# Performance work log

Hardware: AMD Instinct MI355X
Metric: run time of the kernel (lower is better)

## Reference

```python
import jax, jax.numpy as jnp
import numpy as np

N_ATOMS = 20000
N_EDGES = 500000
F = 128


def setup_inputs() -> dict:
    key = jax.random.key(0)
    ks = jax.random.split(key, 10)
    q = jax.random.normal(ks[0], (N_ATOMS, 1, F), dtype=jnp.float32)
    mu = jax.random.normal(ks[1], (N_ATOMS, 3, F), dtype=jnp.float32)
    Wij = jax.random.normal(ks[2], (N_EDGES, 1, 3 * F), dtype=jnp.float32)
    dir_ij = jax.random.normal(ks[3], (N_EDGES, 3), dtype=jnp.float32)
    idx_i = jax.random.randint(ks[4], (N_EDGES,), 0, N_ATOMS)
    idx_j = jax.random.randint(ks[5], (N_EDGES,), 0, N_ATOMS)
    # interatomic_context_net params: Dense(F->F, silu), Dense(F->3F)
    W1 = jax.random.normal(ks[6], (F, F), dtype=jnp.float32) * 0.05
    b1 = jnp.zeros((F,), dtype=jnp.float32)
    W2 = jax.random.normal(ks[7], (F, 3 * F), dtype=jnp.float32) * 0.05
    b2 = jnp.zeros((3 * F,), dtype=jnp.float32)
    return {"q": q, "mu": mu, "Wij": Wij, "dir_ij": dir_ij,
            "idx_i": idx_i, "idx_j": idx_j, "n_atoms": N_ATOMS,
            "W1": W1, "b1": b1, "W2": W2, "b2": b2}


def reference(q, mu, Wij, dir_ij, idx_i, idx_j, n_atoms, W1, b1, W2, b2):
    nb = q.shape[-1]  # n_atom_basis
    # interatomic_context_net: Dense(silu) -> Dense(linear)
    h = jax.nn.silu(jnp.einsum('naf,fg->nag', q, W1) + b1)
    x = jnp.einsum('naf,fg->nag', h, W2) + b2            # [N, 1, 3F]
    # gather to edges, apply radial filter
    x = Wij * x[idx_j]                                   # [E, 1, 3F]
    dq, dmuR, dmumu = jnp.split(x, 3, axis=-1)           # each [E, 1, F]
    dq = jax.ops.segment_sum(dq, idx_i, num_segments=n_atoms)       # [N, 1, F]
    muj = mu[idx_j]                                      # [E, 3, F]
    dmu = dmuR * dir_ij[..., None] + dmumu * muj         # [E, 3, F]
    dmu = jax.ops.segment_sum(dmu, idx_i, num_segments=n_atoms)     # [N, 3, F]
    return q + dq, mu + dmu
```

## Files before the change

### kernel.cpp

```cpp
#include <hip/hip_runtime.h>
#include <hip/hip_bf16.h>

#define N_ATOMS 20000
#define N_EDGES 500000
#define FDIM    128
#define TFDIM   384

__device__ inline float4 ld4(const float* p) { return *(const float4*)p; }
__device__ inline void st4(float* p, float4 v) { *(float4*)p = v; }
__device__ inline float4 mul4(float4 a, float4 b) {
    return make_float4(a.x*b.x, a.y*b.y, a.z*b.z, a.w*b.w);
}
__device__ inline void fma4(float4& acc, float4 a, float4 b) {
    acc.x += a.x*b.x; acc.y += a.y*b.y; acc.z += a.z*b.z; acc.w += a.w*b.w;
}
__device__ inline void fma4s(float4& acc, float4 a, float s) {
    acc.x += a.x*s; acc.y += a.y*s; acc.z += a.z*s; acc.w += a.w*s;
}


__global__ void zero_counts_kernel(int* __restrict__ counts) {
    int i = blockIdx.x * 256 + threadIdx.x;
    if (i < N_ATOMS) counts[i] = 0;
}

__global__ void hist_kernel(const int* __restrict__ idx_i, int* __restrict__ counts) {
    int e = blockIdx.x * 256 + threadIdx.x;
    if (e < N_EDGES) atomicAdd(&counts[idx_i[e]], 1);
}

__global__ __launch_bounds__(1024) void scan_kernel(const int* __restrict__ counts,
                                                    int* __restrict__ offsets,
                                                    int* __restrict__ cursor) {
    __shared__ int ls[1024];
    const int CH = 20;
    int t = threadIdx.x;
    int beg = t * CH;
    int end = beg + CH; if (end > N_ATOMS) end = N_ATOMS;
    int s = 0;
    for (int i = beg; i < end && i < N_ATOMS; ++i) s += counts[i];
    ls[t] = s;
    __syncthreads();
    for (int off = 1; off < 1024; off <<= 1) {
        int v = (t >= off) ? ls[t - off] : 0;
        __syncthreads();
        ls[t] += v;
        __syncthreads();
    }
    int excl = ls[t] - s;
    int run = excl;
    for (int i = beg; i < end && i < N_ATOMS; ++i) {
        offsets[i] = run;
        cursor[i]  = run;
        run += counts[i];
    }
    if (t == 1023) offsets[N_ATOMS] = ls[1023];
}

__global__ void scatter_kernel(const int* __restrict__ idx_i,
                               int* __restrict__ cursor, int* __restrict__ perm) {
    int e = blockIdx.x * 256 + threadIdx.x;
    if (e < N_EDGES) {
        int pos = atomicAdd(&cursor[idx_i[e]], 1);
        perm[pos] = e;
    }
}

__global__ __launch_bounds__(256) void gemm_bias_act(const float* __restrict__ A,
                                                     const float* __restrict__ W,
                                                     const float* __restrict__ bias,
                                                     float* __restrict__ C,
                                                     int M, int Nout, int act) {
    __shared__ float As[64 * 132];
    __shared__ float Bs[128 * 68];
    int tid  = threadIdx.x;
    int row0 = blockIdx.x * 64;
    int col0 = blockIdx.y * 64;

    for (int t = tid; t < 64 * 32; t += 256) {
        int m = t >> 5, k4 = (t & 31) * 4;
        float4 v = make_float4(0.f, 0.f, 0.f, 0.f);
        int gr = row0 + m;
        if (gr < M) v = ld4(A + (size_t)gr * 128 + k4);
        st4(As + m * 132 + k4, v);
    }
    for (int t = tid; t < 128 * 16; t += 256) {
        int k = t >> 4, n4 = (t & 15) * 4;
        st4(Bs + k * 68 + n4, ld4(W + (size_t)k * Nout + col0 + n4));
    }
    __syncthreads();

    int tx = tid & 15, ty = tid >> 4;
    int cc = col0 + tx * 4;
    float4 bv = ld4(bias + cc);
    float4 acc[4];
    acc[0] = bv; acc[1] = bv; acc[2] = bv; acc[3] = bv;

    const float* Ap = As + (ty * 4) * 132;
    for (int k = 0; k < 128; k += 4) {
        float4 a0 = ld4(Ap + 0 * 132 + k);
        float4 a1 = ld4(Ap + 1 * 132 + k);
        float4 a2 = ld4(Ap + 2 * 132 + k);
        float4 a3 = ld4(Ap + 3 * 132 + k);
        float4 b0 = ld4(Bs + (k + 0) * 68 + tx * 4);
        float4 b1 = ld4(Bs + (k + 1) * 68 + tx * 4);
        float4 b2 = ld4(Bs + (k + 2) * 68 + tx * 4);
        float4 b3 = ld4(Bs + (k + 3) * 68 + tx * 4);
        fma4s(acc[0], b0, a0.x); fma4s(acc[0], b1, a0.y); fma4s(acc[0], b2, a0.z); fma4s(acc[0], b3, a0.w);
        fma4s(acc[1], b0, a1.x); fma4s(acc[1], b1, a1.y); fma4s(acc[1], b2, a1.z); fma4s(acc[1], b3, a1.w);
        fma4s(acc[2], b0, a2.x); fma4s(acc[2], b1, a2.y); fma4s(acc[2], b2, a2.z); fma4s(acc[2], b3, a2.w);
        fma4s(acc[3], b0, a3.x); fma4s(acc[3], b1, a3.y); fma4s(acc[3], b2, a3.z); fma4s(acc[3], b3, a3.w);
    }

    #pragma unroll
    for (int mi = 0; mi < 4; ++mi) {
        float4 v = acc[mi];
        if (act) {
            v.x = v.x / (1.0f + __expf(-v.x));
            v.y = v.y / (1.0f + __expf(-v.y));
            v.z = v.z / (1.0f + __expf(-v.z));
            v.w = v.w / (1.0f + __expf(-v.w));
        }
        int gr = row0 + ty * 4 + mi;
        if (gr < M) st4(C + (size_t)gr * Nout + cc, v);
    }
}

__global__ __launch_bounds__(256) void gather_kernel(const float* __restrict__ q,
                                                     const float* __restrict__ mu,
                                                     const float* __restrict__ Wij,
                                                     const float* __restrict__ dir_ij,
                                                     const int* __restrict__ idx_j,
                                                     const int* __restrict__ offsets,
                                                     const int* __restrict__ perm,
                                                     const float* __restrict__ x,
                                                     float* __restrict__ out_q,
                                                     float* __restrict__ out_mu) {
    int l4 = (threadIdx.x & 31) * 4;
    int a  = blockIdx.x * 8 + (threadIdx.x >> 5);

    float4 aq = ld4(q + (size_t)a * FDIM + l4);
    const float* mb = mu + (size_t)a * TFDIM;
    float4 am0 = ld4(mb + l4);
    float4 am1 = ld4(mb + 128 + l4);
    float4 am2 = ld4(mb + 256 + l4);

    int s = offsets[a];
    int t = offsets[a + 1];
    for (int k = s; k < t; ++k) {
        int e = perm[k];
        int j = idx_j[e];
        const float* w  = Wij + (size_t)e * TFDIM;
        const float* xj = x   + (size_t)j * TFDIM;
        const float* mj = mu  + (size_t)j * TFDIM;
        float4 w0 = ld4(w + l4),        x0 = ld4(xj + l4);
        float4 w1 = ld4(w + 128 + l4),  x1 = ld4(xj + 128 + l4);
        float4 w2 = ld4(w + 256 + l4),  x2 = ld4(xj + 256 + l4);
        float dx = dir_ij[3 * (size_t)e + 0];
        float dy = dir_ij[3 * (size_t)e + 1];
        float dz = dir_ij[3 * (size_t)e + 2];
        float4 m0 = ld4(mj + l4);
        float4 m1 = ld4(mj + 128 + l4);
        float4 m2 = ld4(mj + 256 + l4);

        fma4(aq, w0, x0);
        float4 dR = mul4(w1, x1);
        float4 dM = mul4(w2, x2);
        fma4s(am0, dR, dx); fma4(am0, dM, m0);
        fma4s(am1, dR, dy); fma4(am1, dM, m1);
        fma4s(am2, dR, dz); fma4(am2, dM, m2);
    }

    st4(out_q + (size_t)a * FDIM + l4, aq);
    float* ob = out_mu + (size_t)a * TFDIM;
    st4(ob + l4,        am0);
    st4(ob + 128 + l4,  am1);
    st4(ob + 256 + l4,  am2);
}

extern "C" void kernel_launch(void* const* d_in, const int* in_sizes, int n_in,
                              void* d_out, int out_size, void* d_ws, size_t ws_size,
                              hipStream_t stream) {
    const float* q      = (const float*)d_in[0];
    const float* mu     = (const float*)d_in[1];
    const float* Wij    = (const float*)d_in[2];
    const float* dir_ij = (const float*)d_in[3];
    const int*   idx_i  = (const int*)d_in[4];
    const int*   idx_j  = (const int*)d_in[5];
    const float* W1     = (const float*)d_in[7];
    const float* b1     = (const float*)d_in[8];
    const float* W2     = (const float*)d_in[9];
    const float* b2     = (const float*)d_in[10];

    float* out_q  = (float*)d_out;
    float* out_mu = out_q + (size_t)N_ATOMS * FDIM;

    float* xw     = (float*)d_ws;
    float* hw     = xw + (size_t)N_ATOMS * TFDIM;
    int*   counts = (int*)(hw + (size_t)N_ATOMS * FDIM);
    int*   offs   = counts + N_ATOMS;
    int*   cursor = offs + (N_ATOMS + 1);
    int*   perm   = cursor + N_ATOMS;

    const int eblocks = (N_EDGES + 255) / 256;

    zero_counts_kernel<<<(N_ATOMS + 255) / 256, 256, 0, stream>>>(counts);
    hist_kernel<<<eblocks, 256, 0, stream>>>(idx_i, counts);
    scan_kernel<<<1, 1024, 0, stream>>>(counts, offs, cursor);
    scatter_kernel<<<eblocks, 256, 0, stream>>>(idx_i, cursor, perm);

    gemm_bias_act<<<dim3(313, 2), 256, 0, stream>>>(q,  W1, b1, hw, N_ATOMS, 128, 1);
    gemm_bias_act<<<dim3(313, 6), 256, 0, stream>>>(hw, W2, b2, xw, N_ATOMS, 384, 0);

    gather_kernel<<<2500, 256, 0, stream>>>(q, mu, Wij, dir_ij, idx_j, offs, perm,
                                            xw, out_q, out_mu);
}
```

Measured before the change: 1.330 ms.

## Split atom edges across wavefront halves, pack (e,j) pairs, prefetch next edge

The gather kernel now gives each atom a full 64-lane wavefront. The two 32-lane halves process alternating edges and combine their partial sums with a cross-half shuffle at the end. The scatter pass stores (edge, idx_j) pairs so the gather avoids a dependent idx_j lookup, and the next pair is prefetched one iteration ahead. This doubles the memory-level parallelism per atom and shortens the serial index chain, at the cost of twice as many blocks, the shuffle reductions, and some load imbalance when an atom has an odd number of edges.

```diff
diff --git a/kernel.cpp b/kernel.cpp
--- a/kernel.cpp
+++ b/kernel.cpp
@@ -58,11 +58,12 @@
 }
 
 __global__ void scatter_kernel(const int* __restrict__ idx_i,
-                               int* __restrict__ cursor, int* __restrict__ perm) {
+                               const int* __restrict__ idx_j,
+                               int* __restrict__ cursor, int2* __restrict__ perm2) {
     int e = blockIdx.x * 256 + threadIdx.x;
     if (e < N_EDGES) {
         int pos = atomicAdd(&cursor[idx_i[e]], 1);
-        perm[pos] = e;
+        perm2[pos] = make_int2(e, idx_j[e]);
     }
 }
 
@@ -130,35 +131,40 @@
                                                      const float* __restrict__ mu,
                                                      const float* __restrict__ Wij,
                                                      const float* __restrict__ dir_ij,
-                                                     const int* __restrict__ idx_j,
                                                      const int* __restrict__ offsets,
-                                                     const int* __restrict__ perm,
+                                                     const int2* __restrict__ perm2,
                                                      const float* __restrict__ x,
                                                      float* __restrict__ out_q,
                                                      float* __restrict__ out_mu) {
-    int l4 = (threadIdx.x & 31) * 4;
-    int a  = blockIdx.x * 8 + (threadIdx.x >> 5);
-
-    float4 aq = ld4(q + (size_t)a * FDIM + l4);
-    const float* mb = mu + (size_t)a * TFDIM;
-    float4 am0 = ld4(mb + l4);
-    float4 am1 = ld4(mb + 128 + l4);
-    float4 am2 = ld4(mb + 256 + l4);
+    int lane = threadIdx.x & 63;
+    int wid  = threadIdx.x >> 6;
+    int a    = blockIdx.x * 4 + wid;
+    int half = lane >> 5;
+    int l4   = (lane & 31) * 4;
+
+    float4 aq  = make_float4(0.f, 0.f, 0.f, 0.f);
+    float4 am0 = aq, am1 = aq, am2 = aq;
 
     int s = offsets[a];
     int t = offsets[a + 1];
-    for (int k = s; k < t; ++k) {
-        int e = perm[k];
-        int j = idx_j[e];
+    int k = s + half;
+
+    int e = 0, j = 0;
+    if (k < t) { int2 p = perm2[k]; e = p.x; j = p.y; }
+
+    for (; k < t; k += 2) {
+        int kn = k + 2;
+        int2 pn = (kn < t) ? perm2[kn] : make_int2(0, 0);
+
         const float* w  = Wij + (size_t)e * TFDIM;
         const float* xj = x   + (size_t)j * TFDIM;
         const float* mj = mu  + (size_t)j * TFDIM;
-        float4 w0 = ld4(w + l4),        x0 = ld4(xj + l4);
-        float4 w1 = ld4(w + 128 + l4),  x1 = ld4(xj + 128 + l4);
-        float4 w2 = ld4(w + 256 + l4),  x2 = ld4(xj + 256 + l4);
         float dx = dir_ij[3 * (size_t)e + 0];
         float dy = dir_ij[3 * (size_t)e + 1];
         float dz = dir_ij[3 * (size_t)e + 2];
+        float4 w0 = ld4(w + l4),       x0 = ld4(xj + l4);
+        float4 w1 = ld4(w + 128 + l4), x1 = ld4(xj + 128 + l4);
+        float4 w2 = ld4(w + 256 + l4), x2 = ld4(xj + 256 + l4);
         float4 m0 = ld4(mj + l4);
         float4 m1 = ld4(mj + 128 + l4);
         float4 m2 = ld4(mj + 256 + l4);
@@ -169,13 +175,32 @@
         fma4s(am0, dR, dx); fma4(am0, dM, m0);
         fma4s(am1, dR, dy); fma4(am1, dM, m1);
         fma4s(am2, dR, dz); fma4(am2, dM, m2);
-    }
-
-    st4(out_q + (size_t)a * FDIM + l4, aq);
-    float* ob = out_mu + (size_t)a * TFDIM;
-    st4(ob + l4,        am0);
-    st4(ob + 128 + l4,  am1);
-    st4(ob + 256 + l4,  am2);
+
+        e = pn.x; j = pn.y;
+    }
+
+    aq.x  += __shfl_xor(aq.x, 32);  aq.y  += __shfl_xor(aq.y, 32);
+    aq.z  += __shfl_xor(aq.z, 32);  aq.w  += __shfl_xor(aq.w, 32);
+    am0.x += __shfl_xor(am0.x, 32); am0.y += __shfl_xor(am0.y, 32);
+    am0.z += __shfl_xor(am0.z, 32); am0.w += __shfl_xor(am0.w, 32);
+    am1.x += __shfl_xor(am1.x, 32); am1.y += __shfl_xor(am1.y, 32);
+    am1.z += __shfl_xor(am1.z, 32); am1.w += __shfl_xor(am1.w, 32);
+    am2.x += __shfl_xor(am2.x, 32); am2.y += __shfl_xor(am2.y, 32);
+    am2.z += __shfl_xor(am2.z, 32); am2.w += __shfl_xor(am2.w, 32);
+
+    if (half == 0) {
+        float4 qv = ld4(q + (size_t)a * FDIM + l4);
+        st4(out_q + (size_t)a * FDIM + l4,
+            make_float4(qv.x + aq.x, qv.y + aq.y, qv.z + aq.z, qv.w + aq.w));
+        const float* mb = mu + (size_t)a * TFDIM;
+        float* ob = out_mu + (size_t)a * TFDIM;
+        float4 mv0 = ld4(mb + l4);
+        float4 mv1 = ld4(mb + 128 + l4);
+        float4 mv2 = ld4(mb + 256 + l4);
+        st4(ob + l4,       make_float4(mv0.x + am0.x, mv0.y + am0.y, mv0.z + am0.z, mv0.w + am0.w));
+        st4(ob + 128 + l4, make_float4(mv1.x + am1.x, mv1.y + am1.y, mv1.z + am1.z, mv1.w + am1.w));
+        st4(ob + 256 + l4, make_float4(mv2.x + am2.x, mv2.y + am2.y, mv2.z + am2.z, mv2.w + am2.w));
+    }
 }
 
 extern "C" void kernel_launch(void* const* d_in, const int* in_sizes, int n_in,
@@ -200,18 +225,19 @@
     int*   counts = (int*)(hw + (size_t)N_ATOMS * FDIM);
     int*   offs   = counts + N_ATOMS;
     int*   cursor = offs + (N_ATOMS + 1);
-    int*   perm   = cursor + N_ATOMS;
+    int*   pad    = cursor + N_ATOMS;
+    int2*  perm2  = (int2*)(pad + 1);
 
     const int eblocks = (N_EDGES + 255) / 256;
 
     zero_counts_kernel<<<(N_ATOMS + 255) / 256, 256, 0, stream>>>(counts);
     hist_kernel<<<eblocks, 256, 0, stream>>>(idx_i, counts);
     scan_kernel<<<1, 1024, 0, stream>>>(counts, offs, cursor);
-    scatter_kernel<<<eblocks, 256, 0, stream>>>(idx_i, cursor, perm);
+    scatter_kernel<<<eblocks, 256, 0, stream>>>(idx_i, idx_j, cursor, perm2);
 
     gemm_bias_act<<<dim3(313, 2), 256, 0, stream>>>(q,  W1, b1, hw, N_ATOMS, 128, 1);
     gemm_bias_act<<<dim3(313, 6), 256, 0, stream>>>(hw, W2, b2, xw, N_ATOMS, 384, 0);
 
-    gather_kernel<<<2500, 256, 0, stream>>>(q, mu, Wij, dir_ij, idx_j, offs, perm,
+    gather_kernel<<<5000, 256, 0, stream>>>(q, mu, Wij, dir_ij, offs, perm2,
                                             xw, out_q, out_mu);
 }
```

Measured after the change: 1.312 ms. Within noise of the previous version (-1.4%).
